# Kernel tuning notes

Measured on AMD Instinct MI355X. Metric: run time of the kernel, lower is better.

Reference implementation:

```python
import jax, jax.numpy as jnp
import numpy as np

B, S, D = 4, 2048, 1024


def setup_inputs() -> dict:
    key = jax.random.key(0)
    ks = jax.random.split(key, 7)
    s = 1.0 / np.sqrt(D)
    return {
        "x": jax.random.normal(ks[0], (B, S, D), dtype=jnp.float32),
        "Wq": jax.random.normal(ks[1], (D, D), dtype=jnp.float32) * s,
        "bq": jnp.zeros((D,), dtype=jnp.float32),
        "Wk": jax.random.normal(ks[2], (D, D), dtype=jnp.float32) * s,
        "bk": jnp.zeros((D,), dtype=jnp.float32),
        "Wv": jax.random.normal(ks[3], (D, D), dtype=jnp.float32) * s,
        "bv": jnp.zeros((D,), dtype=jnp.float32),
    }


def reference(x, Wq, bq, Wk, bk, Wv, bv):
    # Linear layers: x @ W^T + b (torch nn.Linear convention)
    Q = jnp.einsum("bsd,ed->bse", x, Wq) + bq
    K = jnp.einsum("bsd,ed->bse", x, Wk) + bk
    V = jnp.einsum("bsd,ed->bse", x, Wv) + bv
    scale = 1.0 / (x.shape[-1] ** 0.5)
    scores = jnp.einsum("bse,bte->bst", Q, K) * scale  # [B, S, S]
    attn = jax.nn.softmax(scores, axis=-1)
    out = jnp.einsum("bst,bte->bse", attn, V)
    return out
```

## Files before the change

kernel.cpp:

```cpp
#include <hip/hip_runtime.h>
#include <math.h>


typedef _Float16 f16;
typedef _Float16 f16x8 __attribute__((ext_vector_type(8)));
typedef _Float16 f16x4 __attribute__((ext_vector_type(4)));
typedef float f32x4 __attribute__((ext_vector_type(4)));

__device__ __forceinline__ void glds16(const void* g, const void* l) {
    __builtin_amdgcn_global_load_lds(
        (const __attribute__((address_space(1))) void*)g,
        (__attribute__((address_space(3))) void*)l, 16, 0, 0);
}

__global__ __launch_bounds__(256) void cvt16_kernel(
    const float* __restrict__ in, f16* __restrict__ o, int n4)
{
    int i = blockIdx.x * 256 + threadIdx.x;
    if (i >= n4) return;
    float4 v = ((const float4*)in)[i];
    f16x4 h = { (f16)v.x, (f16)v.y, (f16)v.z, (f16)v.w };
    ((f16x4*)o)[i] = h;
}

__global__ __launch_bounds__(256) void cvtw_kernel(
    const float* __restrict__ Wq, const float* __restrict__ Wk,
    const float* __restrict__ Wv, f16* __restrict__ o, int n4)
{
    int i = blockIdx.x * 256 + threadIdx.x;
    if (i >= n4) return;
    const float* src = (blockIdx.y == 0) ? Wq : (blockIdx.y == 1) ? Wk : Wv;
    float4 v = ((const float4*)src)[i];
    f16x4 h = { (f16)v.x, (f16)v.y, (f16)v.z, (f16)v.w };
    ((f16x4*)(o + (size_t)blockIdx.y * 1024 * 1024))[i] = h;
}

__global__ __launch_bounds__(256) void zero_kernel(float* __restrict__ p, int n)
{
    int i = blockIdx.x * 256 + threadIdx.x;
    if (i < n) p[i] = 0.0f;
}

__device__ __forceinline__ void mfma_core(
    const f16* __restrict__ A, int lda,
    const f16* __restrict__ B, int ldb,
    int K, int m0, int n0, f16* sm, f32x4 acc[4][4])
{
    f16* sA = sm;
    f16* sB = sm + 8192;

    const int tid  = threadIdx.x;
    const int lane = tid & 63;
    const int wave = tid >> 6;
    const int wm = (wave >> 1) * 64;
    const int wn = (wave & 1) * 64;
    const int lr = lane & 15;
    const int kq = lane >> 4;

    const int srow  = wave * 32;
    const int rloc  = lane >> 3;
    const int chunk = (lane & 7) ^ rloc;
    const int gcol  = chunk * 8;

    const f16* gA = A + (size_t)(m0 + srow + rloc) * lda + gcol;
    const f16* gB = B + (size_t)(n0 + srow + rloc) * ldb + gcol;

    f16* lA = sA + srow * 64;
    f16* lB = sB + srow * 64;

    for (int k0 = 0; k0 < K; k0 += 64) {
        #pragma unroll
        for (int p = 0; p < 4; ++p) {
            glds16(gA + k0 + (size_t)(p * 8) * lda, lA + p * 512);
            glds16(gB + k0 + (size_t)(p * 8) * ldb, lB + p * 512);
        }
        __syncthreads();

        #pragma unroll
        for (int kk = 0; kk < 2; ++kk) {
            f16x8 a[4], b[4];
            #pragma unroll
            for (int i = 0; i < 4; ++i) {
                const int ra = wm + i * 16 + lr;
                const int rb = wn + i * 16 + lr;
                const int c  = kk * 4 + kq;
                a[i] = *(const f16x8*)&sA[ra * 64 + ((c ^ (ra & 7)) * 8)];
                b[i] = *(const f16x8*)&sB[rb * 64 + ((c ^ (rb & 7)) * 8)];
            }
            #pragma unroll
            for (int i = 0; i < 4; ++i)
                #pragma unroll
                for (int j = 0; j < 4; ++j)
                    acc[i][j] = __builtin_amdgcn_mfma_f32_16x16x32_f16(a[i], b[j], acc[i][j], 0, 0, 0);
        }
        __syncthreads();
    }
}

__global__ __launch_bounds__(256) void qkv_mfma_kernel(
    const f16* __restrict__ xh, const f16* __restrict__ Wh,
    const float* __restrict__ bq, const float* __restrict__ bk,
    const float* __restrict__ bv,
    f16* __restrict__ Qh, f16* __restrict__ Kh, f16* __restrict__ Vh)
{
    __shared__ __align__(16) f16 smem[16384];
    const int z  = blockIdx.z;
    const int m0 = blockIdx.y * 128;
    const int n0 = blockIdx.x * 128;

    f32x4 acc[4][4];
    #pragma unroll
    for (int i = 0; i < 4; ++i)
        #pragma unroll
        for (int j = 0; j < 4; ++j) acc[i][j] = (f32x4){0.f, 0.f, 0.f, 0.f};

    mfma_core(xh, 1024, Wh + (size_t)z * 1024 * 1024, 1024, 1024, m0, n0, smem, acc);

    const float* bias = (z == 0) ? bq : (z == 1) ? bk : bv;
    const float  sc   = (z == 0) ? 0.03125f : 1.0f;
    f16* C = (z == 0) ? Qh : (z == 1) ? Kh : Vh;
    const int lane = threadIdx.x & 63;
    const int wave = threadIdx.x >> 6;
    const int wm = (wave >> 1) * 64;
    const int wn = (wave & 1) * 64;
    const int col  = lane & 15;
    const int quad = lane >> 4;

    #pragma unroll
    for (int j = 0; j < 4; ++j) {
        const int gn = n0 + wn + j * 16 + col;
        const float bb = bias[gn];
        #pragma unroll
        for (int i = 0; i < 4; ++i)
            #pragma unroll
            for (int r = 0; r < 4; ++r) {
                const int gm = m0 + wm + i * 16 + quad * 4 + r;
                C[(size_t)gm * 1024 + gn] = (f16)((acc[i][j][r] + bb) * sc);
            }
    }
}

__global__ __launch_bounds__(256) void vtrans_kernel(
    const f16* __restrict__ V, f16* __restrict__ Vt)
{
    __shared__ f16 t[64][72];
    const int b  = blockIdx.z;
    const int s0 = blockIdx.x * 64;
    const int d0 = blockIdx.y * 64;
    const int tid = threadIdx.x;

    const int r  = tid >> 3;
    const int c8 = (tid & 7) * 8;
    const f16* src = V + ((size_t)b * 2048 + s0) * 1024 + d0;
    *(f16x8*)&t[r][c8]      = *(const f16x8*)(src + (size_t)r * 1024 + c8);
    *(f16x8*)&t[r + 32][c8] = *(const f16x8*)(src + (size_t)(r + 32) * 1024 + c8);
    __syncthreads();

    const int dl  = tid >> 2;
    const int sl0 = (tid & 3) * 16;
    f16* dst = Vt + ((size_t)b * 1024 + d0 + dl) * 2048 + s0 + sl0;
    f16 buf[16];
    #pragma unroll
    for (int u = 0; u < 16; ++u) buf[u] = t[sl0 + u][dl];
    *(f16x8*)dst       = *(f16x8*)&buf[0];
    *(f16x8*)(dst + 8) = *(f16x8*)&buf[8];
}

__global__ __launch_bounds__(256) void scores_exp_kernel(
    const f16* __restrict__ Qh, const f16* __restrict__ Kh,
    f16* __restrict__ P, float* __restrict__ sums, int r0, int R)
{
    __shared__ __align__(16) f16 smem[16384];
    const int b  = blockIdx.z;
    const int m0 = blockIdx.y * 128;
    const int n0 = blockIdx.x * 128;

    f32x4 acc[4][4];
    #pragma unroll
    for (int i = 0; i < 4; ++i)
        #pragma unroll
        for (int j = 0; j < 4; ++j) acc[i][j] = (f32x4){0.f, 0.f, 0.f, 0.f};

    const size_t ao = ((size_t)b * 2048 + r0) * 1024;
    const size_t bo = (size_t)b * 2048 * 1024;
    mfma_core(Qh + ao, 1024, Kh + bo, 1024, 1024, m0, n0, smem, acc);

    const int lane = threadIdx.x & 63;
    const int wave = threadIdx.x >> 6;
    const int wm = (wave >> 1) * 64;
    const int wn = (wave & 1) * 64;
    const int col  = lane & 15;
    const int quad = lane >> 4;
    f16* C = P + (size_t)b * R * 2048;

    float rp[4][4];
    #pragma unroll
    for (int i = 0; i < 4; ++i)
        #pragma unroll
        for (int r = 0; r < 4; ++r) rp[i][r] = 0.0f;

    #pragma unroll
    for (int i = 0; i < 4; ++i)
        #pragma unroll
        for (int r = 0; r < 4; ++r) {
            const int gm = m0 + wm + i * 16 + quad * 4 + r;
            #pragma unroll
            for (int j = 0; j < 4; ++j) {
                const int gn = n0 + wn + j * 16 + col;
                const f16 p = (f16)__expf(acc[i][j][r]);
                C[(size_t)gm * 2048 + gn] = p;
                rp[i][r] += (float)p;
            }
        }

    #pragma unroll
    for (int i = 0; i < 4; ++i)
        #pragma unroll
        for (int r = 0; r < 4; ++r) {
            float v = rp[i][r];
            v += __shfl_xor(v, 1);
            v += __shfl_xor(v, 2);
            v += __shfl_xor(v, 4);
            v += __shfl_xor(v, 8);
            rp[i][r] = v;
        }
    if (col == 0) {
        #pragma unroll
        for (int i = 0; i < 4; ++i)
            #pragma unroll
            for (int r = 0; r < 4; ++r) {
                const int row = m0 + wm + i * 16 + quad * 4 + r;
                atomicAdd(&sums[b * R + row], rp[i][r]);
            }
    }
}

__global__ __launch_bounds__(256) void pv_mfma_kernel(
    const f16* __restrict__ P, const f16* __restrict__ Vt,
    const float* __restrict__ sums, float* __restrict__ out, int r0, int R)
{
    __shared__ __align__(16) f16 smem[16384];
    const int b  = blockIdx.z;
    const int m0 = blockIdx.y * 128;
    const int n0 = blockIdx.x * 128;

    f32x4 acc[4][4];
    #pragma unroll
    for (int i = 0; i < 4; ++i)
        #pragma unroll
        for (int j = 0; j < 4; ++j) acc[i][j] = (f32x4){0.f, 0.f, 0.f, 0.f};

    const size_t ao = (size_t)b * R * 2048;
    const size_t bo = (size_t)b * 1024 * 2048;
    mfma_core(P + ao, 2048, Vt + bo, 2048, 2048, m0, n0, smem, acc);

    const int lane = threadIdx.x & 63;
    const int wave = threadIdx.x >> 6;
    const int wm = (wave >> 1) * 64;
    const int wn = (wave & 1) * 64;
    const int col  = lane & 15;
    const int quad = lane >> 4;
    float* C = out + ((size_t)b * 2048 + r0) * 1024;

    #pragma unroll
    for (int i = 0; i < 4; ++i)
        #pragma unroll
        for (int r = 0; r < 4; ++r) {
            const int rl = m0 + wm + i * 16 + quad * 4 + r;
            const float inv = 1.0f / sums[b * R + rl];
            #pragma unroll
            for (int j = 0; j < 4; ++j) {
                const int gn = n0 + wn + j * 16 + col;
                C[(size_t)rl * 1024 + gn] = acc[i][j][r] * inv;
            }
        }
}

extern "C" void kernel_launch(void* const* d_in, const int* in_sizes, int n_in,
                              void* d_out, int out_size, void* d_ws, size_t ws_size,
                              hipStream_t stream)
{
    (void)in_sizes; (void)n_in; (void)out_size;
    const int Bn = 4, S = 2048, D = 1024;
    const float* x  = (const float*)d_in[0];
    const float* Wq = (const float*)d_in[1];
    const float* bq = (const float*)d_in[2];
    const float* Wk = (const float*)d_in[3];
    const float* bk = (const float*)d_in[4];
    const float* Wv = (const float*)d_in[5];
    const float* bv = (const float*)d_in[6];
    float* out = (float*)d_out;

    const size_t MB = 1024 * 1024;
    char* w = (char*)d_ws;
    f16*   xh   = (f16*)(w + 0 * MB);
    f16*   Wh3  = (f16*)(w + 16 * MB);
    f16*   Qh   = (f16*)(w + 22 * MB);
    f16*   Kh   = (f16*)(w + 38 * MB);
    f16*   Vh   = (f16*)(w + 54 * MB);
    f16*   Vt   = (f16*)(w + 70 * MB);
    float* sums = (float*)(w + 86 * MB);
    f16*   Pexp;

    int R;
    if      (ws_size >= 120 * MB) { R = 2048; Pexp = (f16*)(w + 87 * MB); }
    else if (ws_size >= 88 * MB)  { R = 1024; Pexp = (f16*)(w + 0 * MB);  }
    else                          { R = 512;  Pexp = (f16*)(w + 0 * MB);  }

    cvt16_kernel<<<dim3(Bn * S * D / 4 / 256), 256, 0, stream>>>(x, xh, Bn * S * D / 4);
    cvtw_kernel<<<dim3(D * D / 4 / 256, 3), 256, 0, stream>>>(Wq, Wk, Wv, Wh3, D * D / 4);

    qkv_mfma_kernel<<<dim3(D / 128, (Bn * S) / 128, 3), 256, 0, stream>>>(
        xh, Wh3, bq, bk, bv, Qh, Kh, Vh);
    vtrans_kernel<<<dim3(S / 64, D / 64, Bn), 256, 0, stream>>>(Vh, Vt);

    for (int r0 = 0; r0 < S; r0 += R) {
        zero_kernel<<<dim3((Bn * R + 255) / 256), 256, 0, stream>>>(sums, Bn * R);
        scores_exp_kernel<<<dim3(S / 128, R / 128, Bn), 256, 0, stream>>>(
            Qh, Kh, Pexp, sums, r0, R);
        pv_mfma_kernel<<<dim3(D / 128, R / 128, Bn), 256, 0, stream>>>(
            Pexp, Vt, sums, out, r0, R);
    }
}
```

Before: 281.3 us.

## Replace LDS-staged GEMM core with direct global-to-register double-buffered loads

Removes the shared-memory tiling in the common MFMA GEMM core. Each wave now loads its A/B fragments straight from global memory into registers, with a two-stage register double buffer, instead of staging 128x64 tiles in LDS behind barriers. This drops LDS traffic and __syncthreads, but tiles are no longer shared across the waves of a block, so each operand row is fetched by two waves and global/L2 traffic rises. The change relies on caches to absorb the extra loads and adds register pressure.

```diff
diff --git a/kernel.cpp b/kernel.cpp
--- a/kernel.cpp
+++ b/kernel.cpp
@@ -6,12 +6,6 @@
 typedef _Float16 f16x8 __attribute__((ext_vector_type(8)));
 typedef _Float16 f16x4 __attribute__((ext_vector_type(4)));
 typedef float f32x4 __attribute__((ext_vector_type(4)));
-
-__device__ __forceinline__ void glds16(const void* g, const void* l) {
-    __builtin_amdgcn_global_load_lds(
-        (const __attribute__((address_space(1))) void*)g,
-        (__attribute__((address_space(3))) void*)l, 16, 0, 0);
-}
 
 __global__ __launch_bounds__(256) void cvt16_kernel(
     const float* __restrict__ in, f16* __restrict__ o, int n4)
@@ -41,59 +35,53 @@
     if (i < n) p[i] = 0.0f;
 }
 
-__device__ __forceinline__ void mfma_core(
+__device__ __forceinline__ void mfma16(f16x8 a[4], f16x8 b[4], f32x4 acc[4][4])
+{
+    #pragma unroll
+    for (int i = 0; i < 4; ++i)
+        #pragma unroll
+        for (int j = 0; j < 4; ++j)
+            acc[i][j] = __builtin_amdgcn_mfma_f32_16x16x32_f16(a[i], b[j], acc[i][j], 0, 0, 0);
+}
+
+template <int K>
+__device__ __forceinline__ void mfma_core_reg(
     const f16* __restrict__ A, int lda,
     const f16* __restrict__ B, int ldb,
-    int K, int m0, int n0, f16* sm, f32x4 acc[4][4])
-{
-    f16* sA = sm;
-    f16* sB = sm + 8192;
-
-    const int tid  = threadIdx.x;
-    const int lane = tid & 63;
-    const int wave = tid >> 6;
+    int m0, int n0, f32x4 acc[4][4])
+{
+    const int lane = threadIdx.x & 63;
+    const int wave = threadIdx.x >> 6;
     const int wm = (wave >> 1) * 64;
     const int wn = (wave & 1) * 64;
     const int lr = lane & 15;
     const int kq = lane >> 4;
 
-    const int srow  = wave * 32;
-    const int rloc  = lane >> 3;
-    const int chunk = (lane & 7) ^ rloc;
-    const int gcol  = chunk * 8;
-
-    const f16* gA = A + (size_t)(m0 + srow + rloc) * lda + gcol;
-    const f16* gB = B + (size_t)(n0 + srow + rloc) * ldb + gcol;
-
-    f16* lA = sA + srow * 64;
-    f16* lB = sB + srow * 64;
-
-    for (int k0 = 0; k0 < K; k0 += 64) {
-        #pragma unroll
-        for (int p = 0; p < 4; ++p) {
-            glds16(gA + k0 + (size_t)(p * 8) * lda, lA + p * 512);
-            glds16(gB + k0 + (size_t)(p * 8) * ldb, lB + p * 512);
-        }
-        __syncthreads();
-
-        #pragma unroll
-        for (int kk = 0; kk < 2; ++kk) {
-            f16x8 a[4], b[4];
+    const f16* pA = A + (size_t)(m0 + wm + lr) * lda + kq * 8;
+    const f16* pB = B + (size_t)(n0 + wn + lr) * ldb + kq * 8;
+
+    f16x8 a0[4], b0[4], a1[4], b1[4];
+    #pragma unroll
+    for (int i = 0; i < 4; ++i) {
+        a0[i] = *(const f16x8*)(pA + (size_t)(i * 16) * lda);
+        b0[i] = *(const f16x8*)(pB + (size_t)(i * 16) * ldb);
+    }
+    #pragma unroll 4
+    for (int k0 = 32; k0 < K; k0 += 64) {
+        #pragma unroll
+        for (int i = 0; i < 4; ++i) {
+            a1[i] = *(const f16x8*)(pA + (size_t)(i * 16) * lda + k0);
+            b1[i] = *(const f16x8*)(pB + (size_t)(i * 16) * ldb + k0);
+        }
+        mfma16(a0, b0, acc);
+        if (k0 + 32 < K) {
             #pragma unroll
             for (int i = 0; i < 4; ++i) {
-                const int ra = wm + i * 16 + lr;
-                const int rb = wn + i * 16 + lr;
-                const int c  = kk * 4 + kq;
-                a[i] = *(const f16x8*)&sA[ra * 64 + ((c ^ (ra & 7)) * 8)];
-                b[i] = *(const f16x8*)&sB[rb * 64 + ((c ^ (rb & 7)) * 8)];
-            }
-            #pragma unroll
-            for (int i = 0; i < 4; ++i)
-                #pragma unroll
-                for (int j = 0; j < 4; ++j)
-                    acc[i][j] = __builtin_amdgcn_mfma_f32_16x16x32_f16(a[i], b[j], acc[i][j], 0, 0, 0);
-        }
-        __syncthreads();
+                a0[i] = *(const f16x8*)(pA + (size_t)(i * 16) * lda + k0 + 32);
+                b0[i] = *(const f16x8*)(pB + (size_t)(i * 16) * ldb + k0 + 32);
+            }
+        }
+        mfma16(a1, b1, acc);
     }
 }
 
@@ -103,7 +91,6 @@
     const float* __restrict__ bv,
     f16* __restrict__ Qh, f16* __restrict__ Kh, f16* __restrict__ Vh)
 {
-    __shared__ __align__(16) f16 smem[16384];
     const int z  = blockIdx.z;
     const int m0 = blockIdx.y * 128;
     const int n0 = blockIdx.x * 128;
@@ -114,7 +101,7 @@
         #pragma unroll
         for (int j = 0; j < 4; ++j) acc[i][j] = (f32x4){0.f, 0.f, 0.f, 0.f};
 
-    mfma_core(xh, 1024, Wh + (size_t)z * 1024 * 1024, 1024, 1024, m0, n0, smem, acc);
+    mfma_core_reg<1024>(xh, 1024, Wh + (size_t)z * 1024 * 1024, 1024, m0, n0, acc);
 
     const float* bias = (z == 0) ? bq : (z == 1) ? bk : bv;
     const float  sc   = (z == 0) ? 0.03125f : 1.0f;
@@ -170,7 +157,6 @@
     const f16* __restrict__ Qh, const f16* __restrict__ Kh,
     f16* __restrict__ P, float* __restrict__ sums, int r0, int R)
 {
-    __shared__ __align__(16) f16 smem[16384];
     const int b  = blockIdx.z;
     const int m0 = blockIdx.y * 128;
     const int n0 = blockIdx.x * 128;
@@ -183,7 +169,7 @@
 
     const size_t ao = ((size_t)b * 2048 + r0) * 1024;
     const size_t bo = (size_t)b * 2048 * 1024;
-    mfma_core(Qh + ao, 1024, Kh + bo, 1024, 1024, m0, n0, smem, acc);
+    mfma_core_reg<1024>(Qh + ao, 1024, Kh + bo, 1024, m0, n0, acc);
 
     const int lane = threadIdx.x & 63;
     const int wave = threadIdx.x >> 6;
@@ -239,7 +225,6 @@
     const f16* __restrict__ P, const f16* __restrict__ Vt,
     const float* __restrict__ sums, float* __restrict__ out, int r0, int R)
 {
-    __shared__ __align__(16) f16 smem[16384];
     const int b  = blockIdx.z;
     const int m0 = blockIdx.y * 128;
     const int n0 = blockIdx.x * 128;
@@ -252,7 +237,7 @@
 
     const size_t ao = (size_t)b * R * 2048;
     const size_t bo = (size_t)b * 1024 * 2048;
-    mfma_core(P + ao, 2048, Vt + bo, 2048, 2048, m0, n0, smem, acc);
+    mfma_core_reg<2048>(P + ao, 2048, Vt + bo, 2048, m0, n0, acc);
 
     const int lane = threadIdx.x & 63;
     const int wave = threadIdx.x >> 6;
```

New measurement: 526.4 us. +87.2%, slower.
